# Optimization experiments

Measured on AMD Instinct MI355X. Metric: run time of the kernel, lower is better.

## Reference

```python
import jax, jax.numpy as jnp
import numpy as np

DIM = 2048
NUM_HEADS = 16
HEAD_DIM = 128


def setup_inputs() -> dict:
    key = jax.random.key(0)
    ks = jax.random.split(key, 9)
    B, S = 2, 2048
    s = lambda fan_in: 1.0 / np.sqrt(fan_in)
    return {
        "x": jax.random.normal(ks[0], (B, S, DIM), dtype=jnp.float32),
        "Wq": jax.random.uniform(ks[1], (DIM, NUM_HEADS * HEAD_DIM), jnp.float32, -s(DIM), s(DIM)),
        "bq": jax.random.uniform(ks[2], (NUM_HEADS * HEAD_DIM,), jnp.float32, -s(DIM), s(DIM)),
        "Wk": jax.random.uniform(ks[3], (DIM, HEAD_DIM), jnp.float32, -s(DIM), s(DIM)),
        "bk": jax.random.uniform(ks[4], (HEAD_DIM,), jnp.float32, -s(DIM), s(DIM)),
        "Wv": jax.random.uniform(ks[5], (DIM, HEAD_DIM), jnp.float32, -s(DIM), s(DIM)),
        "bv": jax.random.uniform(ks[6], (HEAD_DIM,), jnp.float32, -s(DIM), s(DIM)),
        "Wo": jax.random.uniform(ks[7], (NUM_HEADS * HEAD_DIM, DIM), jnp.float32, -s(NUM_HEADS * HEAD_DIM), s(NUM_HEADS * HEAD_DIM)),
        "bo": jax.random.uniform(ks[8], (DIM,), jnp.float32, -s(NUM_HEADS * HEAD_DIM), s(NUM_HEADS * HEAD_DIM)),
    }


def reference(x, Wq, bq, Wk, bk, Wv, bv, Wo, bo):
    B, S, _ = x.shape
    H, D = NUM_HEADS, HEAD_DIM
    q = (x @ Wq + bq).reshape(B, S, H, D)          # bnhd
    k = x @ Wk + bk                                 # bmd (single shared KV head)
    v = x @ Wv + bv                                 # bmd
    scale = 1.0 / np.sqrt(D).astype(np.float32)
    scores = jnp.einsum('bnhd,bmd->bnhm', q, k) * scale  # [B,S,H,S]
    attn = jax.nn.softmax(scores, axis=-1)
    out = jnp.einsum('bnhm,bmd->bnhd', attn, v)
    out = out.reshape(B, S, H * D)
    return out @ Wo + bo
```

## Files before the change

kernel.cpp:

```cpp
#include <hip/hip_runtime.h>
#include <cstdint>


#define SEQ 2048
#define NQKV 2304
#define MTOT 4096

typedef __attribute__((ext_vector_type(8))) short bf16x8;
typedef __attribute__((ext_vector_type(4))) float f32x4;
typedef __attribute__((ext_vector_type(16))) float f32x16;

__device__ __forceinline__ unsigned short cvt_bf16(float f) {
  union { float f; unsigned int u; } v; v.f = f;
  unsigned int r = v.u + 0x7FFFu + ((v.u >> 16) & 1u);
  return (unsigned short)(r >> 16);
}

__device__ __forceinline__ unsigned cvt_pk_bf16(float lo, float hi_) {
  unsigned r;
  asm("v_cvt_pk_bf16_f32 %0, %1, %2" : "=v"(r) : "v"(lo), "v"(hi_));
  return r;
}

__device__ __forceinline__ void plane_swap(unsigned &a, unsigned &b) {
  asm volatile("v_permlane32_swap_b32 %0, %1" : "+v"(a), "+v"(b));
}

__device__ __forceinline__ float exp2_(float x) {
#if __has_builtin(__builtin_amdgcn_exp2f)
  return __builtin_amdgcn_exp2f(x);
#else
  return exp2f(x);
#endif
}

typedef const __attribute__((address_space(1))) void gvoid;
typedef __attribute__((address_space(3))) void lvoid;
__device__ __forceinline__ void gload16(const void* g, void* l) {
  __builtin_amdgcn_global_load_lds((gvoid*)g, (lvoid*)l, 16, 0, 0);
}


__global__ __launch_bounds__(256) void cast_x_kernel(const float* __restrict__ x,
                                                     unsigned short* __restrict__ o) {
  long long i = ((long long)blockIdx.x * 256 + threadIdx.x) * 8;
  float4 a = *(const float4*)(x + i);
  float4 b = *(const float4*)(x + i + 4);
  union { bf16x8 v; unsigned short u[8]; } r;
  r.u[0] = cvt_bf16(a.x); r.u[1] = cvt_bf16(a.y); r.u[2] = cvt_bf16(a.z); r.u[3] = cvt_bf16(a.w);
  r.u[4] = cvt_bf16(b.x); r.u[5] = cvt_bf16(b.y); r.u[6] = cvt_bf16(b.z); r.u[7] = cvt_bf16(b.w);
  *(bf16x8*)(o + i) = r.v;
}

__global__ __launch_bounds__(256) void transpose_cast(
    const float* __restrict__ s0, const float* __restrict__ s1, const float* __restrict__ s2,
    int n1, int n2, int st0, int st1, int st2,
    unsigned short* __restrict__ dst, int K) {
  __shared__ float t[32][33];
  int n0 = blockIdx.x * 32, k0 = blockIdx.y * 32;
  const float* src; int off, stride;
  if (n0 < n1)      { src = s0; off = 0;  stride = st0; }
  else if (n0 < n2) { src = s1; off = n1; stride = st1; }
  else              { src = s2; off = n2; stride = st2; }
  int tx = threadIdx.x & 31, ty = threadIdx.x >> 5;
  #pragma unroll
  for (int r = 0; r < 4; r++)
    t[ty + r * 8][tx] = src[(size_t)(k0 + ty + r * 8) * stride + (n0 - off) + tx];
  __syncthreads();
  #pragma unroll
  for (int r = 0; r < 4; r++)
    dst[(size_t)(n0 + ty + r * 8) * K + k0 + tx] = cvt_bf16(t[tx][ty + r * 8]);
}

__global__ __launch_bounds__(256) void concat_bias(const float* __restrict__ bq,
    const float* __restrict__ bk, const float* __restrict__ bv, float* __restrict__ b1) {
  int i = blockIdx.x * 256 + threadIdx.x;
  if (i < NQKV) b1[i] = (i < 2048) ? bq[i] : (i < 2176 ? bk[i - 2048] : bv[i - 2176]);
}

__global__ __launch_bounds__(256) void kfrag_prep(const unsigned short* __restrict__ qkv,
                                                  unsigned short* __restrict__ kfrag) {
  int gid = blockIdx.x * 4 + (threadIdx.x >> 6);
  int l = threadIdx.x & 63;
  int b = gid >> 9, rem = gid & 511;
  int jt = rem >> 3, kt = rem & 7;
  const unsigned short* src = qkv + (size_t)(b * 2048 + jt * 32 + (l & 31)) * NQKV
                              + 2048 + kt * 16 + (l >> 5) * 8;
  *(bf16x8*)(kfrag + (size_t)gid * 512 + l * 8) = *(const bf16x8*)src;
}

__global__ __launch_bounds__(256) void vfrag_prep(const unsigned short* __restrict__ qkv,
                                                  unsigned short* __restrict__ vfrag) {
  int gid = blockIdx.x * 4 + (threadIdx.x >> 6);
  int l = threadIdx.x & 63;
  int b = gid >> 9, rem = gid & 511;
  int jt = rem >> 3, s = (rem >> 2) & 1, d0 = rem & 3;
  union { bf16x8 v; unsigned short u[8]; } o;
  #pragma unroll
  for (int e = 0; e < 8; e++)
    o.u[e] = qkv[(size_t)(b * 2048 + jt * 32 + s * 16 + (l >> 5) * 8 + e) * NQKV
                 + 2176 + d0 * 32 + (l & 31)];
  *(bf16x8*)(vfrag + (size_t)gid * 512 + l * 8) = o.v;
}

template <int BF16_OUT>
__global__ __launch_bounds__(256) void gemm_bt(const unsigned short* __restrict__ A,
    const unsigned short* __restrict__ BT, const float* __restrict__ bias,
    void* __restrict__ Cout, int N) {
  __shared__ unsigned short As[128 * 32];
  __shared__ unsigned short Bs[128 * 32];
  const int tid = threadIdx.x;
  const int l = tid & 63, w = tid >> 6;
  const int l15 = l & 15, g = l >> 4;
  const int wr = w >> 1, wc = w & 1;
  const int brow = blockIdx.x * 128, bcol = blockIdx.y * 128;
  const int K = 2048;
  const unsigned short* ga = A + (size_t)(brow + w * 32 + (l >> 2)) * K + (l & 3) * 8;
  const unsigned short* gb = BT + (size_t)(bcol + w * 32 + (l >> 2)) * K + (l & 3) * 8;
  unsigned short* lA = &As[w * 1024];
  unsigned short* lB = &Bs[w * 1024];
  f32x4 acc[4][4];
  const f32x4 z = {0.f, 0.f, 0.f, 0.f};
  #pragma unroll
  for (int i = 0; i < 4; i++)
    #pragma unroll
    for (int j = 0; j < 4; j++) acc[i][j] = z;

  for (int kt = 0; kt < K; kt += 32) {
    gload16(ga + kt, lA);
    gload16(ga + kt + 16 * K, lA + 512);
    gload16(gb + kt, lB);
    gload16(gb + kt + 16 * K, lB + 512);
    __syncthreads();
    bf16x8 af[4], bfr[4];
    #pragma unroll
    for (int mi = 0; mi < 4; mi++)
      af[mi] = *(const bf16x8*)&As[(wr * 64 + mi * 16 + l15) * 32 + g * 8];
    #pragma unroll
    for (int ni = 0; ni < 4; ni++)
      bfr[ni] = *(const bf16x8*)&Bs[(wc * 64 + ni * 16 + l15) * 32 + g * 8];
    __syncthreads();
    #pragma unroll
    for (int mi = 0; mi < 4; mi++)
      #pragma unroll
      for (int ni = 0; ni < 4; ni++)
        acc[mi][ni] = __builtin_amdgcn_mfma_f32_16x16x32_bf16(af[mi], bfr[ni], acc[mi][ni], 0, 0, 0);
  }
  float* Cf = (float*)Cout;
  unsigned short* Cb = (unsigned short*)Cout;
  #pragma unroll
  for (int ni = 0; ni < 4; ni++) {
    int col = bcol + wc * 64 + ni * 16 + l15;
    float bv = bias[col];
    #pragma unroll
    for (int mi = 0; mi < 4; mi++) {
      int row = brow + wr * 64 + mi * 16 + g * 4;
      #pragma unroll
      for (int r = 0; r < 4; r++) {
        float v = acc[mi][ni][r] + bv;
        if (BF16_OUT) Cb[(size_t)(row + r) * N + col] = cvt_bf16(v);
        else          Cf[(size_t)(row + r) * N + col] = v;
      }
    }
  }
}

__global__ __launch_bounds__(64, 2) void attn_kernel(
    const unsigned short* __restrict__ qkv, const unsigned short* __restrict__ kfrag,
    const unsigned short* __restrict__ vfrag, unsigned short* __restrict__ aout) {
  const int l = threadIdx.x, l31 = l & 31, hi = l >> 5;
  const int bid = blockIdx.x;
  const int qt = bid & 63, h = (bid >> 6) & 15, b = bid >> 10;
  const float C2 = 0.12752299126446508f;

  bf16x8 qf[8];
  {
    const unsigned short* qp = qkv + (size_t)(b * 2048 + qt * 32 + l31) * NQKV + h * 128 + hi * 8;
    #pragma unroll
    for (int kt = 0; kt < 8; kt++) qf[kt] = *(const bf16x8*)(qp + kt * 16);
  }
  const unsigned short* kp = kfrag + (size_t)b * 262144 + l * 8;
  const unsigned short* vp = vfrag + (size_t)b * 262144 + l * 8;

  f32x16 acc[4];
  #pragma unroll
  for (int d0 = 0; d0 < 4; d0++)
    #pragma unroll
    for (int r = 0; r < 16; r++) acc[d0][r] = 0.f;
  float mrun = -3.0e38f, lsum = 0.f;

  bf16x8 ka[8], kb2[8], vr[8];
  #pragma unroll
  for (int u = 0; u < 8; u++) ka[u] = *(const bf16x8*)(kp + u * 512);

#define ATTN_TILE(KC, KN, jtv)                                                  \
  do {                                                                          \
    const int jn_ = ((jtv) < 63) ? (jtv) + 1 : 63;                              \
    _Pragma("unroll")                                                           \
    for (int u = 0; u < 8; u++)                                                 \
      vr[u] = *(const bf16x8*)(vp + (size_t)(jtv) * 4096 + u * 512);            \
    _Pragma("unroll")                                                           \
    for (int u = 0; u < 8; u++)                                                 \
      KN[u] = *(const bf16x8*)(kp + (size_t)jn_ * 4096 + u * 512);              \
    f32x16 se, so;                                                              \
    _Pragma("unroll")                                                           \
    for (int r = 0; r < 16; r++) { se[r] = 0.f; so[r] = 0.f; }                  \
    _Pragma("unroll")                                                           \
    for (int kt = 0; kt < 4; kt++) {                                            \
      se = __builtin_amdgcn_mfma_f32_32x32x16_bf16(KC[2 * kt], qf[2 * kt], se, 0, 0, 0); \
      so = __builtin_amdgcn_mfma_f32_32x32x16_bf16(KC[2 * kt + 1], qf[2 * kt + 1], so, 0, 0, 0); \
    }                                                                           \
    float stv[16];                                                              \
    float vmax = -3.0e38f;                                                      \
    _Pragma("unroll")                                                           \
    for (int r = 0; r < 16; r++) { stv[r] = se[r] + so[r]; vmax = fmaxf(vmax, stv[r]); } \
    vmax = fmaxf(vmax, __shfl_xor(vmax, 32));                                   \
    if ((jtv) == 0) {                                                           \
      mrun = vmax;                                                              \
    } else if (!__all((vmax - mrun) * C2 <= 8.0f)) {                            \
      float mn_ = fmaxf(mrun, vmax);                                            \
      float al_ = exp2_((mrun - mn_) * C2);                                     \
      mrun = mn_; lsum *= al_;                                                  \
      _Pragma("unroll")                                                         \
      for (int r = 0; r < 16; r++) {                                            \
        float av_ = __shfl(al_, (r & 3) + 8 * (r >> 2) + 4 * hi);               \
        _Pragma("unroll")                                                       \
        for (int d0 = 0; d0 < 4; d0++) acc[d0][r] *= av_;                       \
      }                                                                         \
    }                                                                           \
    const float mc_ = mrun * C2;                                                \
    float rs_ = 0.f;                                                            \
    _Pragma("unroll")                                                           \
    for (int r = 0; r < 16; r++) { stv[r] = exp2_(stv[r] * C2 - mc_); rs_ += stv[r]; } \
    rs_ += __shfl_xor(rs_, 32);                                                 \
    lsum += rs_;                                                                \
    _Pragma("unroll")                                                           \
    for (int s = 0; s < 2; s++) {                                               \
      unsigned a0_ = cvt_pk_bf16(stv[s * 8 + 0], stv[s * 8 + 1]);               \
      unsigned b0_ = cvt_pk_bf16(stv[s * 8 + 4], stv[s * 8 + 5]);               \
      plane_swap(a0_, b0_);                                                     \
      unsigned a1_ = cvt_pk_bf16(stv[s * 8 + 2], stv[s * 8 + 3]);               \
      unsigned b1_ = cvt_pk_bf16(stv[s * 8 + 6], stv[s * 8 + 7]);               \
      plane_swap(a1_, b1_);                                                     \
      union { bf16x8 v; unsigned u[4]; } pa_;                                   \
      pa_.u[0] = a0_; pa_.u[1] = a1_; pa_.u[2] = b0_; pa_.u[3] = b1_;           \
      _Pragma("unroll")                                                         \
      for (int d0 = 0; d0 < 4; d0++)                                            \
        acc[d0] = __builtin_amdgcn_mfma_f32_32x32x16_bf16(pa_.v, vr[s * 4 + d0], acc[d0], 0, 0, 0); \
    }                                                                           \
  } while (0)

  for (int jt2 = 0; jt2 < 32; jt2++) {
    ATTN_TILE(ka, kb2, 2 * jt2);
    ATTN_TILE(kb2, ka, 2 * jt2 + 1);
  }
#undef ATTN_TILE

  float linv = 1.0f / lsum;
  const int qrow0 = b * 2048 + qt * 32;
  #pragma unroll
  for (int r = 0; r < 16; r++) {
    const int crow = (r & 3) + 8 * (r >> 2) + 4 * hi;
    float li = __shfl(linv, crow);
    size_t rbase = (size_t)(qrow0 + crow) * 2048 + h * 128 + l31;
    #pragma unroll
    for (int d0 = 0; d0 < 4; d0++)
      aout[rbase + d0 * 32] = cvt_bf16(acc[d0][r] * li);
  }
}


extern "C" void kernel_launch(void* const* d_in, const int* in_sizes, int n_in,
                              void* d_out, int out_size, void* d_ws, size_t ws_size,
                              hipStream_t stream) {
  const float* x  = (const float*)d_in[0];
  const float* Wq = (const float*)d_in[1];
  const float* bq = (const float*)d_in[2];
  const float* Wk = (const float*)d_in[3];
  const float* bk = (const float*)d_in[4];
  const float* Wv = (const float*)d_in[5];
  const float* bv = (const float*)d_in[6];
  const float* Wo = (const float*)d_in[7];
  const float* bo = (const float*)d_in[8];
  float* out = (float*)d_out;

  char* ws = (char*)d_ws;
  size_t off = 0;
  auto alloc = [&](size_t bytes) -> void* {
    void* p = ws + off;
    off += (bytes + 255) & ~(size_t)255;
    return p;
  };
  unsigned short* xb     = (unsigned short*)alloc((size_t)MTOT * 2048 * 2);
  unsigned short* W1T    = (unsigned short*)alloc((size_t)NQKV * 2048 * 2);
  unsigned short* WoT    = (unsigned short*)alloc((size_t)2048 * 2048 * 2);
  float*          bias1  = (float*)alloc((size_t)NQKV * 4);
  unsigned short* qkv    = (unsigned short*)alloc((size_t)MTOT * NQKV * 2);
  unsigned short* kfragb = (unsigned short*)alloc((size_t)2 * 262144 * 2);
  unsigned short* vfragb = (unsigned short*)alloc((size_t)2 * 262144 * 2);
  unsigned short* aoutb  = (unsigned short*)alloc((size_t)MTOT * 2048 * 2);
  if (off > ws_size) return;

  cast_x_kernel<<<4096, 256, 0, stream>>>(x, xb);
  transpose_cast<<<dim3(72, 64), 256, 0, stream>>>(Wq, Wk, Wv, 2048, 2176,
                                                   2048, 128, 128, W1T, 2048);
  transpose_cast<<<dim3(64, 64), 256, 0, stream>>>(Wo, Wo, Wo, 2048, 2048,
                                                   2048, 2048, 2048, WoT, 2048);
  concat_bias<<<9, 256, 0, stream>>>(bq, bk, bv, bias1);

  gemm_bt<1><<<dim3(32, 18), 256, 0, stream>>>(xb, W1T, bias1, qkv, NQKV);
  kfrag_prep<<<256, 256, 0, stream>>>(qkv, kfragb);
  vfrag_prep<<<256, 256, 0, stream>>>(qkv, vfragb);
  attn_kernel<<<2048, 64, 0, stream>>>(qkv, kfragb, vfragb, aoutb);
  gemm_bt<0><<<dim3(32, 16), 256, 0, stream>>>(aoutb, WoT, bo, out, 2048);
}
```

Measured before the change: 213.8 us.

## Process two 32-row query tiles per attention wave to reuse K/V fragments

Each attention wavefront now handles 64 query rows (two 32-row tiles) instead of 32, so every K and V fragment loaded from global memory feeds twice as many MFMAs. The grid halves to 1024 blocks and launch bounds drop to one block per SIMD to allow the doubled accumulator and Q register footprint. This cuts K/V load traffic per FLOP but lowers occupancy and parallelism, and register pressure may cause spills.

After: 206.8 us. 1.03x faster.

```diff
diff --git a/kernel.cpp b/kernel.cpp
--- a/kernel.cpp
+++ b/kernel.cpp
@@ -165,89 +165,103 @@
   }
 }
 
-__global__ __launch_bounds__(64, 2) void attn_kernel(
+__global__ __launch_bounds__(64, 1) void attn_kernel(
     const unsigned short* __restrict__ qkv, const unsigned short* __restrict__ kfrag,
     const unsigned short* __restrict__ vfrag, unsigned short* __restrict__ aout) {
   const int l = threadIdx.x, l31 = l & 31, hi = l >> 5;
   const int bid = blockIdx.x;
-  const int qt = bid & 63, h = (bid >> 6) & 15, b = bid >> 10;
+  const int qt = bid & 31, h = (bid >> 5) & 15, b = bid >> 9;
   const float C2 = 0.12752299126446508f;
 
-  bf16x8 qf[8];
-  {
-    const unsigned short* qp = qkv + (size_t)(b * 2048 + qt * 32 + l31) * NQKV + h * 128 + hi * 8;
-    #pragma unroll
-    for (int kt = 0; kt < 8; kt++) qf[kt] = *(const bf16x8*)(qp + kt * 16);
+  bf16x8 qf[2][8];
+  #pragma unroll
+  for (int q2 = 0; q2 < 2; q2++) {
+    const unsigned short* qp =
+        qkv + (size_t)(b * 2048 + qt * 64 + q2 * 32 + l31) * NQKV + h * 128 + hi * 8;
+    #pragma unroll
+    for (int kt = 0; kt < 8; kt++) qf[q2][kt] = *(const bf16x8*)(qp + kt * 16);
   }
   const unsigned short* kp = kfrag + (size_t)b * 262144 + l * 8;
   const unsigned short* vp = vfrag + (size_t)b * 262144 + l * 8;
 
-  f32x16 acc[4];
-  #pragma unroll
-  for (int d0 = 0; d0 < 4; d0++)
-    #pragma unroll
-    for (int r = 0; r < 16; r++) acc[d0][r] = 0.f;
-  float mrun = -3.0e38f, lsum = 0.f;
+  f32x16 acc[2][4];
+  #pragma unroll
+  for (int q2 = 0; q2 < 2; q2++)
+    #pragma unroll
+    for (int d0 = 0; d0 < 4; d0++)
+      #pragma unroll
+      for (int r = 0; r < 16; r++) acc[q2][d0][r] = 0.f;
+  float mrun[2] = {-3.0e38f, -3.0e38f}, lsum[2] = {0.f, 0.f};
 
   bf16x8 ka[8], kb2[8], vr[8];
   #pragma unroll
   for (int u = 0; u < 8; u++) ka[u] = *(const bf16x8*)(kp + u * 512);
 
-#define ATTN_TILE(KC, KN, jtv)                                                  \
+#define SOFT_PV(STV, Q2, jtv)                                                   \
   do {                                                                          \
-    const int jn_ = ((jtv) < 63) ? (jtv) + 1 : 63;                              \
-    _Pragma("unroll")                                                           \
-    for (int u = 0; u < 8; u++)                                                 \
-      vr[u] = *(const bf16x8*)(vp + (size_t)(jtv) * 4096 + u * 512);            \
-    _Pragma("unroll")                                                           \
-    for (int u = 0; u < 8; u++)                                                 \
-      KN[u] = *(const bf16x8*)(kp + (size_t)jn_ * 4096 + u * 512);              \
-    f32x16 se, so;                                                              \
-    _Pragma("unroll")                                                           \
-    for (int r = 0; r < 16; r++) { se[r] = 0.f; so[r] = 0.f; }                  \
-    _Pragma("unroll")                                                           \
-    for (int kt = 0; kt < 4; kt++) {                                            \
-      se = __builtin_amdgcn_mfma_f32_32x32x16_bf16(KC[2 * kt], qf[2 * kt], se, 0, 0, 0); \
-      so = __builtin_amdgcn_mfma_f32_32x32x16_bf16(KC[2 * kt + 1], qf[2 * kt + 1], so, 0, 0, 0); \
-    }                                                                           \
-    float stv[16];                                                              \
     float vmax = -3.0e38f;                                                      \
     _Pragma("unroll")                                                           \
-    for (int r = 0; r < 16; r++) { stv[r] = se[r] + so[r]; vmax = fmaxf(vmax, stv[r]); } \
+    for (int r = 0; r < 16; r++) vmax = fmaxf(vmax, STV[r]);                    \
     vmax = fmaxf(vmax, __shfl_xor(vmax, 32));                                   \
     if ((jtv) == 0) {                                                           \
-      mrun = vmax;                                                              \
-    } else if (!__all((vmax - mrun) * C2 <= 8.0f)) {                            \
-      float mn_ = fmaxf(mrun, vmax);                                            \
-      float al_ = exp2_((mrun - mn_) * C2);                                     \
-      mrun = mn_; lsum *= al_;                                                  \
+      mrun[Q2] = vmax;                                                          \
+    } else if (!__all((vmax - mrun[Q2]) * C2 <= 8.0f)) {                        \
+      float mn_ = fmaxf(mrun[Q2], vmax);                                        \
+      float al_ = exp2_((mrun[Q2] - mn_) * C2);                                 \
+      mrun[Q2] = mn_; lsum[Q2] *= al_;                                          \
       _Pragma("unroll")                                                         \
       for (int r = 0; r < 16; r++) {                                            \
         float av_ = __shfl(al_, (r & 3) + 8 * (r >> 2) + 4 * hi);               \
         _Pragma("unroll")                                                       \
-        for (int d0 = 0; d0 < 4; d0++) acc[d0][r] *= av_;                       \
+        for (int d0 = 0; d0 < 4; d0++) acc[Q2][d0][r] *= av_;                   \
       }                                                                         \
     }                                                                           \
-    const float mc_ = mrun * C2;                                                \
+    const float mc_ = mrun[Q2] * C2;                                            \
     float rs_ = 0.f;                                                            \
     _Pragma("unroll")                                                           \
-    for (int r = 0; r < 16; r++) { stv[r] = exp2_(stv[r] * C2 - mc_); rs_ += stv[r]; } \
+    for (int r = 0; r < 16; r++) { STV[r] = exp2_(STV[r] * C2 - mc_); rs_ += STV[r]; } \
     rs_ += __shfl_xor(rs_, 32);                                                 \
-    lsum += rs_;                                                                \
+    lsum[Q2] += rs_;                                                            \
     _Pragma("unroll")                                                           \
     for (int s = 0; s < 2; s++) {                                               \
-      unsigned a0_ = cvt_pk_bf16(stv[s * 8 + 0], stv[s * 8 + 1]);               \
-      unsigned b0_ = cvt_pk_bf16(stv[s * 8 + 4], stv[s * 8 + 5]);               \
+      unsigned a0_ = cvt_pk_bf16(STV[s * 8 + 0], STV[s * 8 + 1]);               \
+      unsigned b0_ = cvt_pk_bf16(STV[s * 8 + 4], STV[s * 8 + 5]);               \
       plane_swap(a0_, b0_);                                                     \
-      unsigned a1_ = cvt_pk_bf16(stv[s * 8 + 2], stv[s * 8 + 3]);               \
-      unsigned b1_ = cvt_pk_bf16(stv[s * 8 + 6], stv[s * 8 + 7]);               \
+      unsigned a1_ = cvt_pk_bf16(STV[s * 8 + 2], STV[s * 8 + 3]);               \
+      unsigned b1_ = cvt_pk_bf16(STV[s * 8 + 6], STV[s * 8 + 7]);               \
       plane_swap(a1_, b1_);                                                     \
       union { bf16x8 v; unsigned u[4]; } pa_;                                   \
       pa_.u[0] = a0_; pa_.u[1] = a1_; pa_.u[2] = b0_; pa_.u[3] = b1_;           \
       _Pragma("unroll")                                                         \
       for (int d0 = 0; d0 < 4; d0++)                                            \
-        acc[d0] = __builtin_amdgcn_mfma_f32_32x32x16_bf16(pa_.v, vr[s * 4 + d0], acc[d0], 0, 0, 0); \
+        acc[Q2][d0] = __builtin_amdgcn_mfma_f32_32x32x16_bf16(pa_.v, vr[s * 4 + d0], acc[Q2][d0], 0, 0, 0); \
     }                                                                           \
+  } while (0)
+
+#define ATTN_TILE(KC, KN, jtv)                                                  \
+  do {                                                                          \
+    const int jn_ = ((jtv) < 63) ? (jtv) + 1 : 63;                              \
+    _Pragma("unroll")                                                           \
+    for (int u = 0; u < 8; u++)                                                 \
+      vr[u] = *(const bf16x8*)(vp + (size_t)(jtv) * 4096 + u * 512);            \
+    _Pragma("unroll")                                                           \
+    for (int u = 0; u < 8; u++)                                                 \
+      KN[u] = *(const bf16x8*)(kp + (size_t)jn_ * 4096 + u * 512);              \
+    f32x16 se0, so0, se1, so1;                                                  \
+    _Pragma("unroll")                                                           \
+    for (int r = 0; r < 16; r++) { se0[r] = 0.f; so0[r] = 0.f; se1[r] = 0.f; so1[r] = 0.f; } \
+    _Pragma("unroll")                                                           \
+    for (int kt = 0; kt < 4; kt++) {                                            \
+      se0 = __builtin_amdgcn_mfma_f32_32x32x16_bf16(KC[2 * kt], qf[0][2 * kt], se0, 0, 0, 0); \
+      so0 = __builtin_amdgcn_mfma_f32_32x32x16_bf16(KC[2 * kt + 1], qf[0][2 * kt + 1], so0, 0, 0, 0); \
+      se1 = __builtin_amdgcn_mfma_f32_32x32x16_bf16(KC[2 * kt], qf[1][2 * kt], se1, 0, 0, 0); \
+      so1 = __builtin_amdgcn_mfma_f32_32x32x16_bf16(KC[2 * kt + 1], qf[1][2 * kt + 1], so1, 0, 0, 0); \
+    }                                                                           \
+    float stv0[16], stv1[16];                                                   \
+    _Pragma("unroll")                                                           \
+    for (int r = 0; r < 16; r++) { stv0[r] = se0[r] + so0[r]; stv1[r] = se1[r] + so1[r]; } \
+    SOFT_PV(stv0, 0, jtv);                                                      \
+    SOFT_PV(stv1, 1, jtv);                                                      \
   } while (0)
 
   for (int jt2 = 0; jt2 < 32; jt2++) {
@@ -255,17 +269,21 @@
     ATTN_TILE(kb2, ka, 2 * jt2 + 1);
   }
 #undef ATTN_TILE
-
-  float linv = 1.0f / lsum;
-  const int qrow0 = b * 2048 + qt * 32;
-  #pragma unroll
-  for (int r = 0; r < 16; r++) {
-    const int crow = (r & 3) + 8 * (r >> 2) + 4 * hi;
-    float li = __shfl(linv, crow);
-    size_t rbase = (size_t)(qrow0 + crow) * 2048 + h * 128 + l31;
-    #pragma unroll
-    for (int d0 = 0; d0 < 4; d0++)
-      aout[rbase + d0 * 32] = cvt_bf16(acc[d0][r] * li);
+#undef SOFT_PV
+
+  #pragma unroll
+  for (int q2 = 0; q2 < 2; q2++) {
+    float linv = 1.0f / lsum[q2];
+    const int qrow0 = b * 2048 + qt * 64 + q2 * 32;
+    #pragma unroll
+    for (int r = 0; r < 16; r++) {
+      const int crow = (r & 3) + 8 * (r >> 2) + 4 * hi;
+      float li = __shfl(linv, crow);
+      size_t rbase = (size_t)(qrow0 + crow) * 2048 + h * 128 + l31;
+      #pragma unroll
+      for (int d0 = 0; d0 < 4; d0++)
+        aout[rbase + d0 * 32] = cvt_bf16(acc[q2][d0][r] * li);
+    }
   }
 }
 
@@ -311,6 +329,6 @@
   gemm_bt<1><<<dim3(32, 18), 256, 0, stream>>>(xb, W1T, bias1, qkv, NQKV);
   kfrag_prep<<<256, 256, 0, stream>>>(qkv, kfragb);
   vfrag_prep<<<256, 256, 0, stream>>>(qkv, vfragb);
-  attn_kernel<<<2048, 64, 0, stream>>>(qkv, kfragb, vfragb, aoutb);
+  attn_kernel<<<1024, 64, 0, stream>>>(qkv, kfragb, vfragb, aoutb);
   gemm_bt<0><<<dim3(32, 16), 256, 0, stream>>>(aoutb, WoT, bo, out, 2048);
 }
```
